# Optimization experiments

Measured on AMD Instinct MI355X. Metric: run time of the kernel, lower is better.

Reference implementation:

```python
import jax, jax.numpy as jnp
import numpy as np

B, S, HID, NH = 2, 2048, 1024, 16
HD = HID // NH
BASE = 10000.0


def _rope_tables(seq_len, head_dim):
    i = jnp.arange(0, head_dim, 2, dtype=jnp.float32)
    theta = BASE ** (-i / head_dim)
    pos = jnp.arange(seq_len, dtype=jnp.float32)
    m_theta = jnp.outer(pos, theta)  # [S, HD/2]
    cos = jnp.repeat(jnp.cos(m_theta), 2, axis=1)  # [S, HD]
    sin = jnp.repeat(jnp.sin(m_theta), 2, axis=1)
    return cos, sin


def _apply_rope(x, cos, sin):
    # x: [B, NH, S, HD]; interleaved rotation: (-x1, x0, -x3, x2, ...)
    x_even = x[..., 0::2]
    x_odd = x[..., 1::2]
    inv_x = jnp.stack((-x_odd, x_even), axis=-1).reshape(x.shape)
    return x * cos[None, None] + inv_x * sin[None, None]


def setup_inputs() -> dict:
    key = jax.random.key(0)
    ks = jax.random.split(key, 7)
    q = jax.random.normal(ks[0], (B, S, HID), dtype=jnp.float32)
    k = jax.random.normal(ks[1], (B, S, HID), dtype=jnp.float32)
    v = jax.random.normal(ks[2], (B, S, HID), dtype=jnp.float32)
    scale = 1.0 / np.sqrt(HID)
    Wq = jax.random.normal(ks[3], (HID, HID), dtype=jnp.float32) * scale
    Wk = jax.random.normal(ks[4], (HID, HID), dtype=jnp.float32) * scale
    Wv = jax.random.normal(ks[5], (HID, HID), dtype=jnp.float32) * scale
    Wo = jax.random.normal(ks[6], (HID, HID), dtype=jnp.float32) * scale
    mask = jnp.triu(jnp.ones((S, S), dtype=bool), k=1)[None, None]  # causal, True = masked
    return {"q": q, "k": k, "v": v, "mask": mask,
            "Wq": Wq, "Wk": Wk, "Wv": Wv, "Wo": Wo}


def reference(q, k, v, mask, Wq, Wk, Wv, Wo):
    cos, sin = _rope_tables(S, HD)
    # Linear (torch stores weight as [out, in]; y = x @ W.T)
    qh = (q @ Wq.T).reshape(B, S, NH, HD).transpose(0, 2, 1, 3)
    kh = (k @ Wk.T).reshape(B, S, NH, HD).transpose(0, 2, 1, 3)
    vh = (v @ Wv.T).reshape(B, S, NH, HD).transpose(0, 2, 1, 3)
    qh = _apply_rope(qh, cos, sin)
    kh = _apply_rope(kh, cos, sin)
    scores = jnp.einsum("bhqd,bhkd->bhqk", qh, kh) / np.sqrt(HD)
    neg_min = jnp.finfo(jnp.float32).min
    scores = jnp.where(mask, neg_min, scores)
    attn = jax.nn.softmax(scores, axis=-1)
    out = jnp.einsum("bhqk,bhkd->bhqd", attn, vh)  # [B,NH,S,HD]
    out = out.transpose(0, 2, 1, 3).reshape(B, S, HID)
    return out @ Wo.T
```

## Files before the change

kernel.cpp:

```cpp
#include <hip/hip_runtime.h>

#define S_LEN 2048
#define HIDN  1024
#define NHEAD 16
#define HDIM  64
#define MROWS 4096
#define KDIM  1024
#define NDIM  1024

typedef __attribute__((ext_vector_type(8))) short bf16x8;
typedef __attribute__((ext_vector_type(4))) float f32x4;

static __device__ __forceinline__ ushort f2bf(float f) {
    unsigned int u = __float_as_uint(f);
    u = (u + 0x7fffu + ((u >> 16) & 1u)) >> 16;
    return (ushort)u;
}
static __device__ __forceinline__ float bf2f(ushort u) {
    return __uint_as_float(((unsigned int)u) << 16);
}

static __device__ __forceinline__ void gload16(const ushort* g, ushort* l) {
    __builtin_amdgcn_global_load_lds(
        (const __attribute__((address_space(1))) unsigned int*)g,
        (__attribute__((address_space(3))) unsigned int*)l, 16, 0, 0);
}

__global__ __launch_bounds__(256) void prep_kernel(
    const float* __restrict__ q, const float* __restrict__ k,
    const float* __restrict__ v, const float* __restrict__ Wq,
    const float* __restrict__ Wk, const float* __restrict__ Wv,
    const float* __restrict__ Wo,
    ushort* __restrict__ qb, ushort* __restrict__ kb, ushort* __restrict__ vb,
    ushort* __restrict__ Wqb, ushort* __restrict__ Wkb, ushort* __restrict__ Wvb,
    ushort* __restrict__ Wob,
    float* __restrict__ rc, float* __restrict__ rs)
{
    const long Q4 = (long)MROWS * KDIM / 4;
    const long W4 = (long)NDIM * KDIM / 4;
    if (blockIdx.x < 16384) {
        long i = (long)blockIdx.x * 256 + threadIdx.x;
        const float* src; ushort* dst; long off;
        if (i < Q4)          { src = q; dst = qb; off = i; }
        else if (i < 2 * Q4) { src = k; dst = kb; off = i - Q4; }
        else if (i < 3 * Q4) { src = v; dst = vb; off = i - 2 * Q4; }
        else {
            long t = i - 3 * Q4;
            int wsel = (int)(t >> 18);
            off = t & (W4 - 1);
            src = (wsel == 0) ? Wq : (wsel == 1) ? Wk : (wsel == 2) ? Wv : Wo;
            dst = (wsel == 0) ? Wqb : (wsel == 1) ? Wkb : (wsel == 2) ? Wvb : Wob;
        }
        float4 vv = ((const float4*)src)[off];
        ushort4 o;
        o.x = f2bf(vv.x); o.y = f2bf(vv.y); o.z = f2bf(vv.z); o.w = f2bf(vv.w);
        ((ushort4*)dst)[off] = o;
    } else {
        int idx = (blockIdx.x - 16384) * 256 + threadIdx.x;
        int s  = idx >> 5;
        int jp = idx & 31;
        float theta = expf(-(float)(2 * jp) * (9.210340371976184f / 64.0f));
        float ang = (float)s * theta;
        float sv, cv;
        sincosf(ang, &sv, &cv);
        rc[idx] = cv;
        rs[idx] = sv;
    }
}

static __device__ __forceinline__ void gemm_mainloop(
    const ushort* __restrict__ A, const ushort* __restrict__ W,
    ushort* As, ushort* Bs, f32x4 (&acc)[2][4],
    int m0, int n0, int tid)
{
    const int lane = tid & 63, wid = tid >> 6;
    const int wm = wid & 1, wn = wid >> 1;
    const int quad = lane >> 4, l15 = lane & 15;

    for (int k0 = 0; k0 < KDIM; k0 += 64) {
        __syncthreads();
#pragma unroll
        for (int rr = 0; rr < 2; ++rr) {
            int sidx = tid + rr * 256;
            int row = sidx >> 3;
            int g = (sidx & 7) ^ (row & 7);
            gload16(A + (size_t)(m0 + row) * KDIM + k0 + g * 8, As + sidx * 8);
        }
#pragma unroll
        for (int rr = 0; rr < 4; ++rr) {
            int sidx = tid + rr * 256;
            int row = sidx >> 3;
            int g = (sidx & 7) ^ (row & 7);
            gload16(W + (size_t)(n0 + row) * KDIM + k0 + g * 8, Bs + sidx * 8);
        }
        __syncthreads();

#pragma unroll
        for (int ks = 0; ks < 2; ++ks) {
            bf16x8 af[2], bfr[4];
#pragma unroll
            for (int i = 0; i < 2; ++i) {
                int row = wm * 32 + i * 16 + l15;
                int gg = ((ks << 2) | quad) ^ (row & 7);
                af[i] = *(const bf16x8*)&As[row * 64 + gg * 8];
            }
#pragma unroll
            for (int j = 0; j < 4; ++j) {
                int row = wn * 64 + j * 16 + l15;
                int gg = ((ks << 2) | quad) ^ (row & 7);
                bfr[j] = *(const bf16x8*)&Bs[row * 64 + gg * 8];
            }
#pragma unroll
            for (int i = 0; i < 2; ++i)
#pragma unroll
                for (int j = 0; j < 4; ++j)
                    acc[i][j] = __builtin_amdgcn_mfma_f32_16x16x32_bf16(
                        af[i], bfr[j], acc[i][j], 0, 0, 0);
        }
    }
}

__global__ __launch_bounds__(256) void gemm_qkv(
    const ushort* __restrict__ qb, const ushort* __restrict__ kb,
    const ushort* __restrict__ vb,
    const ushort* __restrict__ Wqb, const ushort* __restrict__ Wkb,
    const ushort* __restrict__ Wvb,
    ushort* __restrict__ Qh, ushort* __restrict__ Kh, ushort* __restrict__ Vt,
    const float* __restrict__ rc, const float* __restrict__ rs)
{
    __shared__ __align__(16) ushort As[64 * 64];
    __shared__ __align__(16) ushort Bs[128 * 64];

    const int tid = threadIdx.x;
    const int lane = tid & 63, wid = tid >> 6;
    const int wm = wid & 1, wn = wid >> 1;
    const int quad = lane >> 4, l15 = lane & 15;
    const int z = blockIdx.z;

    const ushort* A; const ushort* W; int m0, n0;
    if (z == 2) {
        m0 = ((int)blockIdx.y * 2 + ((int)blockIdx.x >> 5)) * 64;
        n0 = ((int)blockIdx.x & 31) * 128;
        A = Wvb; W = vb;
    } else {
        m0 = blockIdx.x * 64; n0 = blockIdx.y * 128;
        A = (z == 0) ? qb : kb;
        W = (z == 0) ? Wqb : Wkb;
    }

    f32x4 acc[2][4];
#pragma unroll
    for (int i = 0; i < 2; ++i)
#pragma unroll
        for (int j = 0; j < 4; ++j) acc[i][j] = 0.0f;

    gemm_mainloop(A, W, As, Bs, acc, m0, n0, tid);

    if (z != 2) {
        ushort* out = (z == 0) ? Qh : Kh;
        const float scale = (z == 0) ? 0.18033688011112042f : 1.0f;
#pragma unroll
        for (int i = 0; i < 2; ++i)
#pragma unroll
            for (int j = 0; j < 4; ++j)
#pragma unroll
                for (int r = 0; r < 4; ++r) {
                    int m = m0 + wm * 32 + i * 16 + quad * 4 + r;
                    int n = n0 + wn * 64 + j * 16 + l15;
                    float v = acc[i][j][r];
                    int b = m >> 11, s = m & (S_LEN - 1);
                    int h = n >> 6, d = n & 63;
                    int pidx = s * 32 + (d >> 1);
                    float cv = rc[pidx], sv = rs[pidx];
                    float partner = __shfl_xor(v, 1);
                    v = (d & 1) ? (v * cv + partner * sv)
                                : (v * cv - partner * sv);
                    out[((size_t)((b * NHEAD + h) * S_LEN + s)) * HDIM + d] =
                        f2bf(v * scale);
                }
    } else {
#pragma unroll
        for (int i = 0; i < 2; ++i)
#pragma unroll
            for (int j = 0; j < 4; ++j)
#pragma unroll
                for (int r = 0; r < 4; ++r) {
                    int m = m0 + wm * 32 + i * 16 + quad * 4 + r;
                    int n = n0 + wn * 64 + j * 16 + l15;
                    int h = m >> 6, d = m & 63;
                    int b = n >> 11, s = n & (S_LEN - 1);
                    Vt[((size_t)((b * NHEAD + h) * HDIM + d)) * S_LEN + s] =
                        f2bf(acc[i][j][r]);
                }
    }
}

__global__ __launch_bounds__(256) void gemm_out(
    const ushort* __restrict__ O0, const ushort* __restrict__ O1,
    const float* __restrict__ L0, const float* __restrict__ L1,
    const ushort* __restrict__ W, float* __restrict__ out)
{
    __shared__ __align__(16) ushort As[64 * 64];
    __shared__ __align__(16) ushort Bs[128 * 64];

    const int tid = threadIdx.x;
    const int lane = tid & 63, wid = tid >> 6;
    const int wm = wid & 1, wn = wid >> 1;
    const int quad = lane >> 4, l15 = lane & 15;
    const int m0 = blockIdx.x * 64, n0 = blockIdx.y * 128;

    f32x4 acc[2][4];
#pragma unroll
    for (int i = 0; i < 2; ++i)
#pragma unroll
        for (int j = 0; j < 4; ++j) acc[i][j] = 0.0f;

    for (int k0 = 0; k0 < KDIM; k0 += 64) {
        const int h = k0 >> 6;
        bf16x8 a0[2], a1[2];
        float li[2];
#pragma unroll
        for (int rr = 0; rr < 2; ++rr) {
            int sidx = tid + rr * 256;
            int row = sidx >> 3;
            int g = (sidx & 7) ^ (row & 7);
            int m = m0 + row, bb = m >> 11, s = m & (S_LEN - 1);
            size_t rowO = (size_t)(bb * NHEAD + h) * S_LEN + s;
            a0[rr] = *(const bf16x8*)(O0 + rowO * HDIM + g * 8);
            a1[rr] = *(const bf16x8*)(O1 + rowO * HDIM + g * 8);
            li[rr] = __builtin_amdgcn_rcpf(L0[rowO] + L1[rowO]);
        }
        __syncthreads();
#pragma unroll
        for (int rr = 0; rr < 2; ++rr) {
            int sidx = tid + rr * 256;
            bf16x8 packed;
#pragma unroll
            for (int e = 0; e < 8; ++e) {
                float f = (bf2f((ushort)a0[rr][e]) + bf2f((ushort)a1[rr][e])) * li[rr];
                packed[e] = (short)(__float_as_uint(f) >> 16);
            }
            *(bf16x8*)&As[sidx * 8] = packed;
        }
#pragma unroll
        for (int rr = 0; rr < 4; ++rr) {
            int sidx = tid + rr * 256;
            int row = sidx >> 3;
            int g = (sidx & 7) ^ (row & 7);
            gload16(W + (size_t)(n0 + row) * KDIM + k0 + g * 8, Bs + sidx * 8);
        }
        __syncthreads();

#pragma unroll
        for (int ks = 0; ks < 2; ++ks) {
            bf16x8 af[2], bfr[4];
#pragma unroll
            for (int i = 0; i < 2; ++i) {
                int row = wm * 32 + i * 16 + l15;
                int gg = ((ks << 2) | quad) ^ (row & 7);
                af[i] = *(const bf16x8*)&As[row * 64 + gg * 8];
            }
#pragma unroll
            for (int j = 0; j < 4; ++j) {
                int row = wn * 64 + j * 16 + l15;
                int gg = ((ks << 2) | quad) ^ (row & 7);
                bfr[j] = *(const bf16x8*)&Bs[row * 64 + gg * 8];
            }
#pragma unroll
            for (int i = 0; i < 2; ++i)
#pragma unroll
                for (int j = 0; j < 4; ++j)
                    acc[i][j] = __builtin_amdgcn_mfma_f32_16x16x32_bf16(
                        af[i], bfr[j], acc[i][j], 0, 0, 0);
        }
    }

#pragma unroll
    for (int i = 0; i < 2; ++i)
#pragma unroll
        for (int j = 0; j < 4; ++j)
#pragma unroll
            for (int r = 0; r < 4; ++r) {
                int m = m0 + wm * 32 + i * 16 + quad * 4 + r;
                int n = n0 + wn * 64 + j * 16 + l15;
                out[(size_t)m * NDIM + n] = acc[i][j][r];
            }
}

__global__ __launch_bounds__(256) void attn_mfma(
    const ushort* __restrict__ Qh, const ushort* __restrict__ Kh,
    const ushort* __restrict__ Vt,
    ushort* __restrict__ O0, ushort* __restrict__ O1,
    float* __restrict__ L0, float* __restrict__ L1)
{
    __shared__ __align__(16) ushort Ks[64 * 64];
    __shared__ __align__(16) ushort Vs[64 * 64];
    __shared__ __align__(16) ushort Ps[64 * 72];

    const int tid = threadIdx.x;
    const int lane = tid & 63, w = tid >> 6;
    const int quad = lane >> 4, l15 = lane & 15;
    const int id = blockIdx.x;
    const int h = id & 15, b = (id >> 4) & 1, t = id >> 5;

    int seg, y;
    if (t < 32) { seg = (t & 1) ? 0 : 1; y = (t & 1) ? 31 - (t >> 1) : (t >> 1); }
    else { int u = t - 32; seg = (u & 1) ? 0 : 1;
           y = (u & 1) ? 15 - (u >> 1) : 16 + (u >> 1); }

    const int qt = seg ? (31 - y) : y;
    const int lo = seg ? ((33 - y) >> 1) : 0;
    const int hi = seg ? (32 - y) : ((y + 2) >> 1);
    const int q0 = qt * 64;
    const size_t hoff = (size_t)(b * NHEAD + h) * S_LEN * HDIM;

    bf16x8 ones;
#pragma unroll
    for (int i = 0; i < 8; ++i) ones[i] = (short)0x3F80;

    bf16x8 qf[2];
#pragma unroll
    for (int ks = 0; ks < 2; ++ks)
        qf[ks] = *(const bf16x8*)(Qh + hoff +
            (size_t)(q0 + w * 16 + l15) * HDIM + ks * 32 + quad * 8);

    f32x4 Oa[4];
    f32x4 Lacc = 0.0f;
#pragma unroll
    for (int j = 0; j < 4; ++j) Oa[j] = 0.0f;

    const int rowq = q0 + w * 16 + quad * 4;

    const ushort* kg[2]; const ushort* vg[2];
#pragma unroll
    for (int rr = 0; rr < 2; ++rr) {
        int sidx = tid + rr * 256;
        int row = sidx >> 3;
        int gsw = (sidx & 7) ^ (row & 7);
        kg[rr] = Kh + hoff + (size_t)(lo * 64 + row) * HDIM + gsw * 8;
        vg[rr] = Vt + hoff + (size_t)row * S_LEN + lo * 64 + gsw * 8;
    }
    ushort* psw = Ps + (w * 16 + quad * 4) * 72;
    const ushort* psr = Ps + (w * 16 + l15) * 72;

    for (int kt = lo; kt < hi; ++kt) {
        const int k0 = kt * 64;
        const bool diag = (kt == qt);
        __syncthreads();
#pragma unroll
        for (int rr = 0; rr < 2; ++rr) {
            int sidx = tid + rr * 256;
            gload16(kg[rr], Ks + sidx * 8);
            gload16(vg[rr], Vs + sidx * 8);
            kg[rr] += 64 * HDIM;
            vg[rr] += 64;
        }
        __syncthreads();

        f32x4 Sa[4];
#pragma unroll
        for (int j = 0; j < 4; ++j) Sa[j] = 0.0f;
#pragma unroll
        for (int ks = 0; ks < 2; ++ks) {
            const int p = ((ks << 2) | quad) ^ (l15 & 7);
            bf16x8 kf[4];
#pragma unroll
            for (int j = 0; j < 4; ++j)
                kf[j] = *(const bf16x8*)&Ks[(j * 16 + l15) * 64 + p * 8];
#pragma unroll
            for (int j = 0; j < 4; ++j)
                Sa[j] = __builtin_amdgcn_mfma_f32_16x16x32_bf16(qf[ks], kf[j],
                                                                Sa[j], 0, 0, 0);
        }

#pragma unroll
        for (int j = 0; j < 4; ++j) {
#pragma unroll
            for (int r = 0; r < 4; ++r) {
                float p = __builtin_amdgcn_exp2f(Sa[j][r]);
                if (diag) {
                    int key = k0 + j * 16 + l15;
                    if (key > rowq + r) p = 0.f;
                }
                psw[r * 72 + j * 16 + l15] = (ushort)(__float_as_uint(p) >> 16);
            }
        }

#pragma unroll
        for (int ks = 0; ks < 2; ++ks) {
            const int p = ((ks << 2) | quad) ^ (l15 & 7);
            bf16x8 pf = *(const bf16x8*)&psr[ks * 32 + quad * 8];
            bf16x8 vf[4];
#pragma unroll
            for (int j = 0; j < 4; ++j)
                vf[j] = *(const bf16x8*)&Vs[(j * 16 + l15) * 64 + p * 8];
#pragma unroll
            for (int j = 0; j < 4; ++j)
                Oa[j] = __builtin_amdgcn_mfma_f32_16x16x32_bf16(pf, vf[j],
                                                                Oa[j], 0, 0, 0);
            Lacc = __builtin_amdgcn_mfma_f32_16x16x32_bf16(pf, ones, Lacc, 0, 0, 0);
        }
    }

    ushort* Op = seg ? O1 : O0;
    float*  Lp = seg ? L1 : L0;
    const size_t rbase = ((size_t)(b * NHEAD + h) * S_LEN + rowq);
#pragma unroll
    for (int r = 0; r < 4; ++r) {
#pragma unroll
        for (int j = 0; j < 4; ++j)
            Op[(rbase + r) * HDIM + j * 16 + l15] = f2bf(Oa[j][r]);
        if (l15 == 0) Lp[rbase + r] = Lacc[r];
    }
}

extern "C" void kernel_launch(void* const* d_in, const int* in_sizes, int n_in,
                              void* d_out, int out_size, void* d_ws, size_t ws_size,
                              hipStream_t stream) {
    const float* qf  = (const float*)d_in[0];
    const float* kf  = (const float*)d_in[1];
    const float* vf  = (const float*)d_in[2];
    const float* Wqf = (const float*)d_in[4];
    const float* Wkf = (const float*)d_in[5];
    const float* Wvf = (const float*)d_in[6];
    const float* Wof = (const float*)d_in[7];
    float* out = (float*)d_out;

    char* wsp = (char*)d_ws;
    float* rc = (float*)wsp;            wsp += 65536 * 4;
    float* rs = (float*)wsp;            wsp += 65536 * 4;
    ushort* qb  = (ushort*)wsp;         wsp += (size_t)MROWS * KDIM * 2;
    ushort* kb  = (ushort*)wsp;         wsp += (size_t)MROWS * KDIM * 2;
    ushort* vb  = (ushort*)wsp;         wsp += (size_t)MROWS * KDIM * 2;
    ushort* Wqb = (ushort*)wsp;         wsp += (size_t)NDIM * KDIM * 2;
    ushort* Wkb = (ushort*)wsp;         wsp += (size_t)NDIM * KDIM * 2;
    ushort* Wvb = (ushort*)wsp;         wsp += (size_t)NDIM * KDIM * 2;
    ushort* Wob = (ushort*)wsp;         wsp += (size_t)NDIM * KDIM * 2;
    ushort* Qh  = (ushort*)wsp;         wsp += (size_t)MROWS * HIDN * 2;
    ushort* Kh  = (ushort*)wsp;         wsp += (size_t)MROWS * HIDN * 2;
    ushort* Vt  = (ushort*)wsp;

    ushort* O0 = qb;
    ushort* O1 = kb;
    float*  L0 = (float*)vb;
    float*  L1 = (float*)vb + 65536;

    prep_kernel<<<16640, 256, 0, stream>>>(qf, kf, vf, Wqf, Wkf, Wvf, Wof,
                                           qb, kb, vb, Wqb, Wkb, Wvb, Wob, rc, rs);

    gemm_qkv<<<dim3(64, 8, 3), 256, 0, stream>>>(
        qb, kb, vb, Wqb, Wkb, Wvb, Qh, Kh, Vt, rc, rs);

    attn_mfma<<<2048, 256, 0, stream>>>(Qh, Kh, Vt, O0, O1, L0, L1);

    gemm_out<<<dim3(64, 8), 256, 0, stream>>>(O0, O1, L0, L1, Wob, out);
}
```

Baseline: 213.3 us.

## Keep attention probabilities in registers via transposed MFMA, drop LDS P staging

Computes S^T by swapping the MFMA operands, so each lane's exponentiated scores already form the B-operand layout of a 16x16x16 bf16 MFMA for the PV product. This removes the shared-memory round trip for P and the extra ones-MFMA for the row sum. The row sum is instead accumulated in scalar registers and reduced with cross-lane shuffles. The trade is twice as many smaller MFMAs for PV, 8-byte V reads from LDS, and a transposed output layout written as ushort4 stores.

```diff
diff --git a/kernel.cpp b/kernel.cpp
--- a/kernel.cpp
+++ b/kernel.cpp
@@ -9,6 +9,7 @@
 #define NDIM  1024
 
 typedef __attribute__((ext_vector_type(8))) short bf16x8;
+typedef __attribute__((ext_vector_type(4))) short bf16x4;
 typedef __attribute__((ext_vector_type(4))) float f32x4;
 
 static __device__ __forceinline__ ushort f2bf(float f) {
@@ -295,7 +296,6 @@
 {
     __shared__ __align__(16) ushort Ks[64 * 64];
     __shared__ __align__(16) ushort Vs[64 * 64];
-    __shared__ __align__(16) ushort Ps[64 * 72];
 
     const int tid = threadIdx.x;
     const int lane = tid & 63, w = tid >> 6;
@@ -314,10 +314,6 @@
     const int q0 = qt * 64;
     const size_t hoff = (size_t)(b * NHEAD + h) * S_LEN * HDIM;
 
-    bf16x8 ones;
-#pragma unroll
-    for (int i = 0; i < 8; ++i) ones[i] = (short)0x3F80;
-
     bf16x8 qf[2];
 #pragma unroll
     for (int ks = 0; ks < 2; ++ks)
@@ -325,11 +321,10 @@
             (size_t)(q0 + w * 16 + l15) * HDIM + ks * 32 + quad * 8);
 
     f32x4 Oa[4];
-    f32x4 Lacc = 0.0f;
-#pragma unroll
-    for (int j = 0; j < 4; ++j) Oa[j] = 0.0f;
-
-    const int rowq = q0 + w * 16 + quad * 4;
+#pragma unroll
+    for (int mt = 0; mt < 4; ++mt) Oa[mt] = 0.0f;
+    float lsum = 0.f;
+    const int myq = q0 + w * 16 + l15;
 
     const ushort* kg[2]; const ushort* vg[2];
 #pragma unroll
@@ -340,8 +335,6 @@
         kg[rr] = Kh + hoff + (size_t)(lo * 64 + row) * HDIM + gsw * 8;
         vg[rr] = Vt + hoff + (size_t)row * S_LEN + lo * 64 + gsw * 8;
     }
-    ushort* psw = Ps + (w * 16 + quad * 4) * 72;
-    const ushort* psr = Ps + (w * 16 + l15) * 72;
 
     for (int kt = lo; kt < hi; ++kt) {
         const int k0 = kt * 64;
@@ -359,59 +352,61 @@
 
         f32x4 Sa[4];
 #pragma unroll
-        for (int j = 0; j < 4; ++j) Sa[j] = 0.0f;
+        for (int jm = 0; jm < 4; ++jm) Sa[jm] = 0.0f;
 #pragma unroll
         for (int ks = 0; ks < 2; ++ks) {
             const int p = ((ks << 2) | quad) ^ (l15 & 7);
             bf16x8 kf[4];
 #pragma unroll
-            for (int j = 0; j < 4; ++j)
-                kf[j] = *(const bf16x8*)&Ks[(j * 16 + l15) * 64 + p * 8];
-#pragma unroll
-            for (int j = 0; j < 4; ++j)
-                Sa[j] = __builtin_amdgcn_mfma_f32_16x16x32_bf16(qf[ks], kf[j],
-                                                                Sa[j], 0, 0, 0);
-        }
-
-#pragma unroll
-        for (int j = 0; j < 4; ++j) {
+            for (int jm = 0; jm < 4; ++jm)
+                kf[jm] = *(const bf16x8*)&Ks[(jm * 16 + l15) * 64 + p * 8];
+#pragma unroll
+            for (int jm = 0; jm < 4; ++jm)
+                Sa[jm] = __builtin_amdgcn_mfma_f32_16x16x32_bf16(kf[jm], qf[ks],
+                                                                 Sa[jm], 0, 0, 0);
+        }
+
+        bf16x4 pb[4];
+#pragma unroll
+        for (int jm = 0; jm < 4; ++jm) {
 #pragma unroll
             for (int r = 0; r < 4; ++r) {
-                float p = __builtin_amdgcn_exp2f(Sa[j][r]);
+                float pv = __builtin_amdgcn_exp2f(Sa[jm][r]);
                 if (diag) {
-                    int key = k0 + j * 16 + l15;
-                    if (key > rowq + r) p = 0.f;
+                    int key = k0 + jm * 16 + quad * 4 + r;
+                    if (key > myq) pv = 0.f;
                 }
-                psw[r * 72 + j * 16 + l15] = (ushort)(__float_as_uint(p) >> 16);
-            }
-        }
-
-#pragma unroll
-        for (int ks = 0; ks < 2; ++ks) {
-            const int p = ((ks << 2) | quad) ^ (l15 & 7);
-            bf16x8 pf = *(const bf16x8*)&psr[ks * 32 + quad * 8];
-            bf16x8 vf[4];
-#pragma unroll
-            for (int j = 0; j < 4; ++j)
-                vf[j] = *(const bf16x8*)&Vs[(j * 16 + l15) * 64 + p * 8];
-#pragma unroll
-            for (int j = 0; j < 4; ++j)
-                Oa[j] = __builtin_amdgcn_mfma_f32_16x16x32_bf16(pf, vf[j],
-                                                                Oa[j], 0, 0, 0);
-            Lacc = __builtin_amdgcn_mfma_f32_16x16x32_bf16(pf, ones, Lacc, 0, 0, 0);
-        }
-    }
+                lsum += pv;
+                pb[jm][r] = (short)(__float_as_uint(pv) >> 16);
+            }
+        }
+
+#pragma unroll
+        for (int jm = 0; jm < 4; ++jm) {
+            const int off = (((jm * 2 + (quad >> 1)) ^ (l15 & 7)) << 3) + (quad & 1) * 4;
+#pragma unroll
+            for (int mt = 0; mt < 4; ++mt) {
+                bf16x4 vf = *(const bf16x4*)&Vs[(mt * 16 + l15) * 64 + off];
+                Oa[mt] = __builtin_amdgcn_mfma_f32_16x16x16bf16_1k(vf, pb[jm],
+                                                                   Oa[mt], 0, 0, 0);
+            }
+        }
+    }
+
+    lsum += __shfl_xor(lsum, 16);
+    lsum += __shfl_xor(lsum, 32);
 
     ushort* Op = seg ? O1 : O0;
     float*  Lp = seg ? L1 : L0;
-    const size_t rbase = ((size_t)(b * NHEAD + h) * S_LEN + rowq);
-#pragma unroll
-    for (int r = 0; r < 4; ++r) {
-#pragma unroll
-        for (int j = 0; j < 4; ++j)
-            Op[(rbase + r) * HDIM + j * 16 + l15] = f2bf(Oa[j][r]);
-        if (l15 == 0) Lp[rbase + r] = Lacc[r];
-    }
+    const size_t row = (size_t)(b * NHEAD + h) * S_LEN + myq;
+#pragma unroll
+    for (int mt = 0; mt < 4; ++mt) {
+        ushort4 o;
+        o.x = f2bf(Oa[mt][0]); o.y = f2bf(Oa[mt][1]);
+        o.z = f2bf(Oa[mt][2]); o.w = f2bf(Oa[mt][3]);
+        *(ushort4*)&Op[row * HDIM + mt * 16 + quad * 4] = o;
+    }
+    if (quad == 0) Lp[row] = lsum;
 }
 
 extern "C" void kernel_launch(void* const* d_in, const int* in_sizes, int n_in,
```

Result: no change. 212.1 us (-0.6%).
